# Optimization experiments

Measured on AMD Instinct MI355X. Metric: run time of the kernel, lower is better.

Reference implementation:

```python
import jax, jax.numpy as jnp
import numpy as np

E, K, IN_DIM, OUT_DIM = 100000, 16, 128, 128


def _linear_init(key, out_d, in_d):
    kw, kb = jax.random.split(key)
    bound = 1.0 / np.sqrt(in_d)
    W = jax.random.uniform(kw, (out_d, in_d), minval=-bound, maxval=bound, dtype=jnp.float32)
    b = jax.random.uniform(kb, (out_d,), minval=-bound, maxval=bound, dtype=jnp.float32)
    return W, b


def setup_inputs() -> dict:
    key = jax.random.key(0)
    k_feat, k_adj, k1, k2, k3, k4 = jax.random.split(key, 6)
    edge_features = jax.random.normal(k_feat, (E, IN_DIM), dtype=jnp.float32)
    edge_adjacency = jax.random.randint(k_adj, (E, K), 0, E, dtype=jnp.int64)
    mW1, mb1 = _linear_init(k1, OUT_DIM, 2 * IN_DIM)
    mW2, mb2 = _linear_init(k2, OUT_DIM, OUT_DIM)
    uW1, ub1 = _linear_init(k3, OUT_DIM, IN_DIM + OUT_DIM)
    uW2, ub2 = _linear_init(k4, OUT_DIM, OUT_DIM)
    return {"edge_features": edge_features, "edge_adjacency": edge_adjacency,
            "mW1": mW1, "mb1": mb1, "mW2": mW2, "mb2": mb2,
            "uW1": uW1, "ub1": ub1, "uW2": ub2 * 0 + ub2 if False else uW1 * 0 + uW1 if False else uW1, "ub1_": ub1} if False else {
            "edge_features": edge_features, "edge_adjacency": edge_adjacency,
            "mW1": mW1, "mb1": mb1, "mW2": mW2, "mb2": mb2,
            "uW1": uW1, "ub1": ub1, "uW2": uW2, "ub2": ub2}


def reference(edge_features, edge_adjacency, mW1, mb1, mW2, mb2, uW1, ub1, uW2, ub2):
    D = edge_features.shape[1]
    # message_net first Linear on concat([feat_i, feat_j]) split into two halves
    # to avoid materializing the [E, K, 2D] concat tensor.
    Wi, Wj = mW1[:, :D], mW1[:, D:]                      # each [O, D]
    self_part = edge_features @ Wi.T                     # [E, O]
    nbr_feat = edge_features[edge_adjacency]             # [E, K, D] gather
    h = jax.nn.relu(self_part[:, None, :] + jnp.einsum('ekd,od->eko', nbr_feat, Wj) + mb1)
    msg = jnp.einsum('eko,po->ekp', h, mW2) + mb2        # [E, K, O]
    msg = msg.mean(axis=1)                               # mean over neighbors -> [E, O]
    # update_net on concat([feat_i, msg_i]), split likewise
    Ui, Um = uW1[:, :D], uW1[:, D:]
    u = jax.nn.relu(edge_features @ Ui.T + msg @ Um.T + ub1)
    return u @ uW2.T + ub2                               # [E, O]
```

## Files before the change

kernel.cpp:

```cpp
#include <hip/hip_runtime.h>
#include <hip/hip_bf16.h>

#define NE 100000
#define NK 16
#define ND 128
#define NTILES 6250
#define NSUP 3125

typedef __bf16 bf16_t;
typedef bf16_t bf16x8 __attribute__((ext_vector_type(8)));
typedef bf16_t bf16x4 __attribute__((ext_vector_type(4)));
typedef float f32x4 __attribute__((ext_vector_type(4)));
typedef float f32x2 __attribute__((ext_vector_type(2)));
typedef unsigned u32x2 __attribute__((ext_vector_type(2)));
typedef unsigned short u16;
typedef unsigned char u8;

__device__ __forceinline__ u16 f2bf(float f) {
  bf16_t h = (bf16_t)f;
  return __builtin_bit_cast(u16, h);
}

__device__ __forceinline__ void soft_barrier() {
  asm volatile("s_waitcnt lgkmcnt(0)" ::: "memory");
  __builtin_amdgcn_s_barrier();
}

__global__ void k_prep(const float* __restrict__ mW1, const float* __restrict__ uW1,
                       const float* __restrict__ uW2, const float* __restrict__ mW2,
                       const float* __restrict__ ub1, const float* __restrict__ mb2,
                       u16* __restrict__ Wi_b, u16* __restrict__ Wj_b,
                       u16* __restrict__ Ui_b, u16* __restrict__ Wp_b,
                       u16* __restrict__ W2_b, float* __restrict__ bp)
{
  const int o = blockIdx.x, t = threadIdx.x;
  Wi_b[o * ND + t] = f2bf(mW1[o * 256 + t]);
  Wj_b[o * ND + t] = f2bf(mW1[o * 256 + 128 + t]);
  Ui_b[o * ND + t] = f2bf(uW1[o * 256 + t]);
  W2_b[o * ND + t] = f2bf(uW2[o * ND + t]);
  float acc = 0.f;
  for (int p = 0; p < 128; ++p)
    acc += uW1[o * 256 + 128 + p] * mW2[p * 128 + t];
  Wp_b[o * ND + t] = f2bf(acc);
  if (t == 0) {
    float b = ub1[o];
    for (int p = 0; p < 128; ++p) b += uW1[o * 256 + 128 + p] * mb2[p];
    bp[o] = b;
  }
}

__global__ __launch_bounds__(512) void k1_szt(
    const float* __restrict__ X, const u16* __restrict__ Wi_b,
    const u16* __restrict__ Wj_b, const u16* __restrict__ Ui_b,
    const float* __restrict__ mb1, const float* __restrict__ bp,
    u8* __restrict__ Sf8, u8* __restrict__ Zf8, u16* __restrict__ Tp)
{
  __shared__ u16 xt[2][16 * ND];
  __shared__ u8  eS[2][16 * ND];
  __shared__ u8  eZ[2][16 * ND];
  __shared__ u16 eT[2][16 * ND];
  const int tid = threadIdx.x, wid = tid >> 6, lane = tid & 63;
  const int r = lane & 15, q = lane >> 4;

  bf16x8 wiF[4], wjF[4], uiF[4];
  f32x4 mbF, bpF;
  {
    const int row = wid * 16 + r;
#pragma unroll
    for (int kk = 0; kk < 4; ++kk) {
      wiF[kk] = *(const bf16x8*)(Wi_b + row * ND + kk * 32 + q * 8);
      wjF[kk] = *(const bf16x8*)(Wj_b + row * ND + kk * 32 + q * 8);
      uiF[kk] = *(const bf16x8*)(Ui_b + row * ND + kk * 32 + q * 8);
    }
    mbF = *(const f32x4*)(mb1 + wid * 16 + q * 4);
    bpF = *(const f32x4*)(bp  + wid * 16 + q * 4);
  }

  const int rs = tid >> 5, cs = tid & 31;
  const int stb = rs * 256 + ((((cs >> 1) ^ (rs & 15)) << 4) | ((cs & 1) << 3));
  const int ewb = r * 256 + ((((wid * 2 + (q >> 1)) ^ (r & 15)) << 4) | ((q & 1) << 3));
  const int ezb = r * 128 + (((wid ^ (r & 7)) << 4) | (q * 4));
  const int erow = tid >> 5, c8 = tid & 31;
  const int erb = erow * 256 + ((((c8 >> 1) ^ (erow & 15)) << 4) | ((c8 & 1) << 3));
  const int zrb = erow * 128 + ((((c8 >> 2) ^ (erow & 7)) << 4) | ((c8 & 3) << 2));

  const long stride = gridDim.x;
  long t = blockIdx.x;
  if (t >= NTILES) return;

  f32x4 xr;
  auto gload = [&](long tt) {
    xr = *(const f32x4*)(X + (tt * 16 + rs) * ND + cs * 4);
  };
  auto stage = [&](int bb) {
    bf16x4 b;
#pragma unroll
    for (int i = 0; i < 4; ++i) b[i] = (bf16_t)xr[i];
    *(bf16x4*)((char*)xt[bb] + stb) = b;
  };

  gload(t);
  stage(0);
  {
    const long t1 = t + stride;
    if (t1 < NTILES) gload(t1);
  }
  soft_barrier();
  int b = 0;

  for (; t < NTILES; t += stride) {
    const long tn = t + stride, tn2 = tn + stride;

    bf16x8 xf[4];
#pragma unroll
    for (int kk = 0; kk < 4; ++kk)
      xf[kk] = *(const bf16x8*)((const char*)xt[b] +
               r * 256 + (((kk * 4 + q) ^ (r & 15)) << 4));

    if (tn < NTILES) stage(b ^ 1);
    if (tn2 < NTILES) gload(tn2);

    f32x4 aS = {0.f, 0.f, 0.f, 0.f};
    f32x4 aZ = {0.f, 0.f, 0.f, 0.f};
    f32x4 aT = {0.f, 0.f, 0.f, 0.f};
#pragma unroll
    for (int kk = 0; kk < 4; ++kk) {
      aS = __builtin_amdgcn_mfma_f32_16x16x32_bf16(wiF[kk], xf[kk], aS, 0, 0, 0);
      aZ = __builtin_amdgcn_mfma_f32_16x16x32_bf16(wjF[kk], xf[kk], aZ, 0, 0, 0);
      aT = __builtin_amdgcn_mfma_f32_16x16x32_bf16(uiF[kk], xf[kk], aT, 0, 0, 0);
    }

    bf16x4 pT;
#pragma unroll
    for (int i = 0; i < 4; ++i) pT[i] = (bf16_t)(aT[i] + bpF[i]);
    unsigned spk = 0, zpk = 0;
    spk = __builtin_amdgcn_cvt_pk_fp8_f32(aS[0] + mbF[0], aS[1] + mbF[1], spk, false);
    spk = __builtin_amdgcn_cvt_pk_fp8_f32(aS[2] + mbF[2], aS[3] + mbF[3], spk, true);
    zpk = __builtin_amdgcn_cvt_pk_fp8_f32(aZ[0], aZ[1], zpk, false);
    zpk = __builtin_amdgcn_cvt_pk_fp8_f32(aZ[2], aZ[3], zpk, true);
    *(unsigned*)((char*)eS[b] + ezb) = spk;
    *(unsigned*)((char*)eZ[b] + ezb) = zpk;
    *(bf16x4*)((char*)eT[b] + ewb) = pT;

    soft_barrier();

    {
      const long e = t * 16 + erow;
      const unsigned vS = *(const unsigned*)((const char*)eS[b] + zrb);
      const unsigned vZ = *(const unsigned*)((const char*)eZ[b] + zrb);
      const bf16x4 vT = *(const bf16x4*)((const char*)eT[b] + erb);
      *(unsigned*)(Sf8 + e * ND + c8 * 4) = vS;
      *(unsigned*)(Zf8 + e * ND + c8 * 4) = vZ;
      *(bf16x4*)(Tp + t * 2048 + erow * 128 + c8 * 4) = vT;
    }
    b ^= 1;
  }
}

__global__ __launch_bounds__(512) void k23_fused(
    const u8* __restrict__ Zf8, const u8* __restrict__ Sf8,
    const int* __restrict__ adj, const u16* __restrict__ Tp,
    const u16* __restrict__ Wp_b, const u16* __restrict__ W2_b,
    const float* __restrict__ ub2, float* __restrict__ out)
{
  __shared__ u16 ht[32 * ND];
  __shared__ u16 tt[32 * ND];
  __shared__ u16 ut[32 * ND];
  const int tid = threadIdx.x, wid = tid >> 6, lane = tid & 63;
  const int r = lane & 15, q = lane >> 4;
  const int ew = wid * 4 + q;
  const int c0 = r * 8;

  bf16x8 wpF[4], w2F[4];
  f32x4 ubF;
  {
    const int row = wid * 16 + r;
#pragma unroll
    for (int kk = 0; kk < 4; ++kk) {
      wpF[kk] = *(const bf16x8*)(Wp_b + row * ND + kk * 32 + q * 8);
      w2F[kk] = *(const bf16x8*)(W2_b + row * ND + kk * 32 + q * 8);
    }
    ubF = *(const f32x4*)(ub2 + wid * 16 + q * 4);
  }

  const int hwb = ew * 256 + ((r ^ (ew & 15)) << 4);
  const int trow = tid >> 4, tch = tid & 15;
  const int twb = trow * 256 + ((tch ^ (trow & 15)) << 4);
  const int uwb0 = (((wid * 2 + (q >> 1)) ^ r) << 4) | ((q & 1) << 3);

  const long stride = gridDim.x;
  long s = blockIdx.x;
  if (s >= NSUP) return;

  auto adjload = [&](long ss) { return adj[(ss * 32 + ew) * NK + r]; };

  int myidxN;
  float hacc[8];
  bf16x8 trC;
  {
    const int myidxC = adjload(s);
    const unsigned* sp = (const unsigned*)(Sf8 + (s * 32 + ew) * ND + c0);
    const unsigned sw0 = sp[0], sw1 = sp[1];
    trC = *(const bf16x8*)(Tp + s * 4096 + trow * 128 + tch * 8);
    const long s1 = s + stride;
    myidxN = (s1 < NSUP) ? adjload(s1) : 0;

    const f32x2 a0 = __builtin_amdgcn_cvt_pk_f32_fp8(sw0, false);
    const f32x2 a1 = __builtin_amdgcn_cvt_pk_f32_fp8(sw0, true);
    const f32x2 a2 = __builtin_amdgcn_cvt_pk_f32_fp8(sw1, false);
    const f32x2 a3 = __builtin_amdgcn_cvt_pk_f32_fp8(sw1, true);
    const float sv[8] = {a0[0], a0[1], a1[0], a1[1], a2[0], a2[1], a3[0], a3[1]};
#pragma unroll
    for (int i = 0; i < 8; ++i) hacc[i] = 0.f;
#pragma unroll
    for (int k = 0; k < NK; ++k) {
      const int n = __shfl(myidxC, (lane & 48) + k);
      const u32x2 zw = *(const u32x2*)(Zf8 + (long)n * ND + c0);
      const f32x2 z0 = __builtin_amdgcn_cvt_pk_f32_fp8(zw[0], false);
      const f32x2 z1 = __builtin_amdgcn_cvt_pk_f32_fp8(zw[0], true);
      const f32x2 z2 = __builtin_amdgcn_cvt_pk_f32_fp8(zw[1], false);
      const f32x2 z3 = __builtin_amdgcn_cvt_pk_f32_fp8(zw[1], true);
      hacc[0] += fmaxf(sv[0] + z0[0], 0.f);
      hacc[1] += fmaxf(sv[1] + z0[1], 0.f);
      hacc[2] += fmaxf(sv[2] + z1[0], 0.f);
      hacc[3] += fmaxf(sv[3] + z1[1], 0.f);
      hacc[4] += fmaxf(sv[4] + z2[0], 0.f);
      hacc[5] += fmaxf(sv[5] + z2[1], 0.f);
      hacc[6] += fmaxf(sv[6] + z3[0], 0.f);
      hacc[7] += fmaxf(sv[7] + z3[1], 0.f);
    }
  }

  for (; s < NSUP; s += stride) {
    const long sn = s + stride, sn2 = sn + stride;
    const bool hasN = (sn < NSUP);

    {
      bf16x8 hv;
#pragma unroll
      for (int i = 0; i < 8; ++i) hv[i] = (bf16_t)(hacc[i] * 0.0625f);
      *(bf16x8*)((char*)ht + hwb) = hv;
      *(bf16x8*)((char*)tt + twb) = trC;
    }

    u32x2 zbufA[8], zbufB[8];
    unsigned swn0 = 0, swn1 = 0;
    bf16x8 trN = {};
    int myidxN2 = 0;
    if (hasN) {
#pragma unroll
      for (int k = 0; k < 8; ++k) {
        const int n = __shfl(myidxN, (lane & 48) + k);
        zbufA[k] = *(const u32x2*)(Zf8 + (long)n * ND + c0);
      }
      const unsigned* sp = (const unsigned*)(Sf8 + (sn * 32 + ew) * ND + c0);
      swn0 = sp[0]; swn1 = sp[1];
      trN = *(const bf16x8*)(Tp + sn * 4096 + trow * 128 + tch * 8);
      if (sn2 < NSUP) myidxN2 = adjload(sn2);
    }

    soft_barrier();

#pragma unroll
    for (int t2 = 0; t2 < 2; ++t2) {
      const int rowb = (t2 * 16 + r) * 256;
      bf16x8 hf[4];
#pragma unroll
      for (int kk = 0; kk < 4; ++kk)
        hf[kk] = *(const bf16x8*)((const char*)ht + rowb + (((kk * 4 + q) ^ r) << 4));
      f32x4 acc;
      {
        const bf16x4 tv = *(const bf16x4*)((const char*)tt + rowb + uwb0);
#pragma unroll
        for (int i = 0; i < 4; ++i) acc[i] = (float)tv[i];
      }
#pragma unroll
      for (int kk = 0; kk < 4; ++kk)
        acc = __builtin_amdgcn_mfma_f32_16x16x32_bf16(wpF[kk], hf[kk], acc, 0, 0, 0);
      bf16x4 u;
#pragma unroll
      for (int i = 0; i < 4; ++i) u[i] = (bf16_t)fmaxf(acc[i], 0.f);
      *(bf16x4*)((char*)ut + rowb + uwb0) = u;
    }

    if (hasN) {
#pragma unroll
      for (int k = 0; k < 8; ++k) {
        const int n = __shfl(myidxN, (lane & 48) + 8 + k);
        zbufB[k] = *(const u32x2*)(Zf8 + (long)n * ND + c0);
      }
    }

    soft_barrier();

#pragma unroll
    for (int t2 = 0; t2 < 2; ++t2) {
      const int rowb = (t2 * 16 + r) * 256;
      bf16x8 uf[4];
#pragma unroll
      for (int kk = 0; kk < 4; ++kk)
        uf[kk] = *(const bf16x8*)((const char*)ut + rowb + (((kk * 4 + q) ^ r) << 4));
      f32x4 o = {0.f, 0.f, 0.f, 0.f};
#pragma unroll
      for (int kk = 0; kk < 4; ++kk)
        o = __builtin_amdgcn_mfma_f32_16x16x32_bf16(w2F[kk], uf[kk], o, 0, 0, 0);
#pragma unroll
      for (int i = 0; i < 4; ++i) o[i] += ubF[i];
      *(f32x4*)(out + (s * 32 + t2 * 16 + r) * ND + wid * 16 + q * 4) = o;
    }

    if (hasN) {
      const f32x2 a0 = __builtin_amdgcn_cvt_pk_f32_fp8(swn0, false);
      const f32x2 a1 = __builtin_amdgcn_cvt_pk_f32_fp8(swn0, true);
      const f32x2 a2 = __builtin_amdgcn_cvt_pk_f32_fp8(swn1, false);
      const f32x2 a3 = __builtin_amdgcn_cvt_pk_f32_fp8(swn1, true);
      const float sv[8] = {a0[0], a0[1], a1[0], a1[1], a2[0], a2[1], a3[0], a3[1]};
#pragma unroll
      for (int i = 0; i < 8; ++i) hacc[i] = 0.f;
#pragma unroll
      for (int k = 0; k < 16; ++k) {
        const u32x2 zw = (k < 8) ? zbufA[k] : zbufB[k - 8];
        const f32x2 z0 = __builtin_amdgcn_cvt_pk_f32_fp8(zw[0], false);
        const f32x2 z1 = __builtin_amdgcn_cvt_pk_f32_fp8(zw[0], true);
        const f32x2 z2 = __builtin_amdgcn_cvt_pk_f32_fp8(zw[1], false);
        const f32x2 z3 = __builtin_amdgcn_cvt_pk_f32_fp8(zw[1], true);
        hacc[0] += fmaxf(sv[0] + z0[0], 0.f);
        hacc[1] += fmaxf(sv[1] + z0[1], 0.f);
        hacc[2] += fmaxf(sv[2] + z1[0], 0.f);
        hacc[3] += fmaxf(sv[3] + z1[1], 0.f);
        hacc[4] += fmaxf(sv[4] + z2[0], 0.f);
        hacc[5] += fmaxf(sv[5] + z2[1], 0.f);
        hacc[6] += fmaxf(sv[6] + z3[0], 0.f);
        hacc[7] += fmaxf(sv[7] + z3[1], 0.f);
      }
      myidxN = myidxN2;
      trC = trN;
    }
  }
}

extern "C" void kernel_launch(void* const* d_in, const int* in_sizes, int n_in,
                              void* d_out, int out_size, void* d_ws, size_t ws_size,
                              hipStream_t stream)
{
  (void)in_sizes; (void)n_in; (void)out_size; (void)ws_size;
  const float* X   = (const float*)d_in[0];
  const int*   adj = (const int*)d_in[1];
  const float* mW1 = (const float*)d_in[2];
  const float* mb1 = (const float*)d_in[3];
  const float* mW2 = (const float*)d_in[4];
  const float* mb2 = (const float*)d_in[5];
  const float* uW1 = (const float*)d_in[6];
  const float* ub1 = (const float*)d_in[7];
  const float* uW2 = (const float*)d_in[8];
  const float* ub2 = (const float*)d_in[9];
  float* out = (float*)d_out;

  u8* ws8  = (u8*)d_ws;
  u8* Sf8  = ws8;
  u8* Zf8  = Sf8 + (size_t)NE * ND;
  u16* Tp  = (u16*)(Zf8 + (size_t)NE * ND);
  u16* Wi_b = Tp + (size_t)NE * ND;
  u16* Wj_b = Wi_b + 128 * 128;
  u16* Ui_b = Wj_b + 128 * 128;
  u16* Wp_b = Ui_b + 128 * 128;
  u16* W2_b = Wp_b + 128 * 128;
  float* bp = (float*)(W2_b + 128 * 128);

  k_prep<<<128, 128, 0, stream>>>(mW1, uW1, uW2, mW2, ub1, mb2,
                                  Wi_b, Wj_b, Ui_b, Wp_b, W2_b, bp);

  k1_szt<<<1024, 512, 0, stream>>>(X, Wi_b, Wj_b, Ui_b, mb1, bp, Sf8, Zf8, Tp);

  k23_fused<<<1024, 512, 0, stream>>>(Zf8, Sf8, adj, Tp, Wp_b, W2_b, ub2, out);
}
```

Before: 87.54 us.

## Store T in MFMA fragment layout, drop LDS staging, split gather buffers

The producer kernel now writes the T tensor already permuted into the MFMA accumulator layout. The fused kernel can then load each lane's T fragment straight from global memory and no longer stages it through a shared-memory tile, which removes one LDS array and its write/read traffic. The neighbour gather is restructured to use a single 8-entry buffer that is consumed in two halves, lowering register pressure, and the accumulation is vectorised into f32x4. Launch bounds are set to 6 waves per SIMD and the grid drops to 768 blocks for occupancy, at the risk of different latency hiding and a permuted-layout correctness dependency between the two kernels.

```diff
diff --git a/kernel.cpp b/kernel.cpp
--- a/kernel.cpp
+++ b/kernel.cpp
@@ -24,6 +24,35 @@
 __device__ __forceinline__ void soft_barrier() {
   asm volatile("s_waitcnt lgkmcnt(0)" ::: "memory");
   __builtin_amdgcn_s_barrier();
+}
+
+__device__ __forceinline__ void unpack_s(unsigned w0, unsigned w1,
+                                         f32x4& sA, f32x4& sB) {
+  const f32x2 a0 = __builtin_amdgcn_cvt_pk_f32_fp8(w0, false);
+  const f32x2 a1 = __builtin_amdgcn_cvt_pk_f32_fp8(w0, true);
+  const f32x2 a2 = __builtin_amdgcn_cvt_pk_f32_fp8(w1, false);
+  const f32x2 a3 = __builtin_amdgcn_cvt_pk_f32_fp8(w1, true);
+  sA[0] = a0[0]; sA[1] = a0[1]; sA[2] = a1[0]; sA[3] = a1[1];
+  sB[0] = a2[0]; sB[1] = a2[1]; sB[2] = a3[0]; sB[3] = a3[1];
+}
+
+__device__ __forceinline__ void acc8(f32x4& hA, f32x4& hB,
+                                     const f32x4 sA, const f32x4 sB,
+                                     const u32x2 zw) {
+  const f32x2 z0 = __builtin_amdgcn_cvt_pk_f32_fp8(zw[0], false);
+  const f32x2 z1 = __builtin_amdgcn_cvt_pk_f32_fp8(zw[0], true);
+  const f32x2 z2 = __builtin_amdgcn_cvt_pk_f32_fp8(zw[1], false);
+  const f32x2 z3 = __builtin_amdgcn_cvt_pk_f32_fp8(zw[1], true);
+  f32x4 vA = sA, vB = sB;
+  vA[0] += z0[0]; vA[1] += z0[1]; vA[2] += z1[0]; vA[3] += z1[1];
+  vB[0] += z2[0]; vB[1] += z2[1]; vB[2] += z3[0]; vB[3] += z3[1];
+#pragma unroll
+  for (int i = 0; i < 4; ++i) {
+    vA[i] = fmaxf(vA[i], 0.f);
+    vB[i] = fmaxf(vB[i], 0.f);
+  }
+  hA += vA;
+  hB += vB;
 }
 
 __global__ void k_prep(const float* __restrict__ mW1, const float* __restrict__ uW1,
@@ -83,6 +112,8 @@
   const int erow = tid >> 5, c8 = tid & 31;
   const int erb = erow * 256 + ((((c8 >> 1) ^ (erow & 15)) << 4) | ((c8 & 1) << 3));
   const int zrb = erow * 128 + ((((c8 >> 2) ^ (erow & 7)) << 4) | ((c8 & 3) << 2));
+  const int trb2 = (tid & 15) * 256 +
+                   ((((tid >> 5) ^ (tid & 15)) << 4) | (((tid >> 4) & 1) << 3));
 
   const long stride = gridDim.x;
   long t = blockIdx.x;
@@ -148,23 +179,22 @@
       const long e = t * 16 + erow;
       const unsigned vS = *(const unsigned*)((const char*)eS[b] + zrb);
       const unsigned vZ = *(const unsigned*)((const char*)eZ[b] + zrb);
-      const bf16x4 vT = *(const bf16x4*)((const char*)eT[b] + erb);
+      const bf16x4 vT = *(const bf16x4*)((const char*)eT[b] + trb2);
       *(unsigned*)(Sf8 + e * ND + c8 * 4) = vS;
       *(unsigned*)(Zf8 + e * ND + c8 * 4) = vZ;
-      *(bf16x4*)(Tp + t * 2048 + erow * 128 + c8 * 4) = vT;
+      *(bf16x4*)(Tp + t * 2048 + tid * 4) = vT;
     }
     b ^= 1;
   }
 }
 
-__global__ __launch_bounds__(512) void k23_fused(
+__global__ __launch_bounds__(512, 6) void k23_fused(
     const u8* __restrict__ Zf8, const u8* __restrict__ Sf8,
     const int* __restrict__ adj, const u16* __restrict__ Tp,
     const u16* __restrict__ Wp_b, const u16* __restrict__ W2_b,
     const float* __restrict__ ub2, float* __restrict__ out)
 {
   __shared__ u16 ht[32 * ND];
-  __shared__ u16 tt[32 * ND];
   __shared__ u16 ut[32 * ND];
   const int tid = threadIdx.x, wid = tid >> 6, lane = tid & 63;
   const int r = lane & 15, q = lane >> 4;
@@ -184,9 +214,8 @@
   }
 
   const int hwb = ew * 256 + ((r ^ (ew & 15)) << 4);
-  const int trow = tid >> 4, tch = tid & 15;
-  const int twb = trow * 256 + ((tch ^ (trow & 15)) << 4);
   const int uwb0 = (((wid * 2 + (q >> 1)) ^ r) << 4) | ((q & 1) << 3);
+  const int tpo = wid * 256 + q * 64 + r * 4;
 
   const long stride = gridDim.x;
   long s = blockIdx.x;
@@ -195,40 +224,33 @@
   auto adjload = [&](long ss) { return adj[(ss * 32 + ew) * NK + r]; };
 
   int myidxN;
-  float hacc[8];
-  bf16x8 trC;
+  f32x4 haccA = {0.f, 0.f, 0.f, 0.f}, haccB = {0.f, 0.f, 0.f, 0.f};
+  bf16x4 trC0, trC1;
   {
     const int myidxC = adjload(s);
     const unsigned* sp = (const unsigned*)(Sf8 + (s * 32 + ew) * ND + c0);
     const unsigned sw0 = sp[0], sw1 = sp[1];
-    trC = *(const bf16x8*)(Tp + s * 4096 + trow * 128 + tch * 8);
-    const long s1 = s + stride;
-    myidxN = (s1 < NSUP) ? adjload(s1) : 0;
-
-    const f32x2 a0 = __builtin_amdgcn_cvt_pk_f32_fp8(sw0, false);
-    const f32x2 a1 = __builtin_amdgcn_cvt_pk_f32_fp8(sw0, true);
-    const f32x2 a2 = __builtin_amdgcn_cvt_pk_f32_fp8(sw1, false);
-    const f32x2 a3 = __builtin_amdgcn_cvt_pk_f32_fp8(sw1, true);
-    const float sv[8] = {a0[0], a0[1], a1[0], a1[1], a2[0], a2[1], a3[0], a3[1]};
-#pragma unroll
-    for (int i = 0; i < 8; ++i) hacc[i] = 0.f;
-#pragma unroll
-    for (int k = 0; k < NK; ++k) {
+    trC0 = *(const bf16x4*)(Tp + s * 4096 + tpo);
+    trC1 = *(const bf16x4*)(Tp + s * 4096 + 2048 + tpo);
+    myidxN = (s + stride < NSUP) ? adjload(s + stride) : 0;
+
+    f32x4 sA, sB;
+    unpack_s(sw0, sw1, sA, sB);
+    u32x2 zb[8];
+#pragma unroll
+    for (int k = 0; k < 8; ++k) {
       const int n = __shfl(myidxC, (lane & 48) + k);
-      const u32x2 zw = *(const u32x2*)(Zf8 + (long)n * ND + c0);
-      const f32x2 z0 = __builtin_amdgcn_cvt_pk_f32_fp8(zw[0], false);
-      const f32x2 z1 = __builtin_amdgcn_cvt_pk_f32_fp8(zw[0], true);
-      const f32x2 z2 = __builtin_amdgcn_cvt_pk_f32_fp8(zw[1], false);
-      const f32x2 z3 = __builtin_amdgcn_cvt_pk_f32_fp8(zw[1], true);
-      hacc[0] += fmaxf(sv[0] + z0[0], 0.f);
-      hacc[1] += fmaxf(sv[1] + z0[1], 0.f);
-      hacc[2] += fmaxf(sv[2] + z1[0], 0.f);
-      hacc[3] += fmaxf(sv[3] + z1[1], 0.f);
-      hacc[4] += fmaxf(sv[4] + z2[0], 0.f);
-      hacc[5] += fmaxf(sv[5] + z2[1], 0.f);
-      hacc[6] += fmaxf(sv[6] + z3[0], 0.f);
-      hacc[7] += fmaxf(sv[7] + z3[1], 0.f);
-    }
+      zb[k] = *(const u32x2*)(Zf8 + (long)n * ND + c0);
+    }
+#pragma unroll
+    for (int k = 0; k < 8; ++k) acc8(haccA, haccB, sA, sB, zb[k]);
+#pragma unroll
+    for (int k = 0; k < 8; ++k) {
+      const int n = __shfl(myidxC, (lane & 48) + 8 + k);
+      zb[k] = *(const u32x2*)(Zf8 + (long)n * ND + c0);
+    }
+#pragma unroll
+    for (int k = 0; k < 8; ++k) acc8(haccA, haccB, sA, sB, zb[k]);
   }
 
   for (; s < NSUP; s += stride) {
@@ -238,25 +260,28 @@
     {
       bf16x8 hv;
 #pragma unroll
-      for (int i = 0; i < 8; ++i) hv[i] = (bf16_t)(hacc[i] * 0.0625f);
+      for (int i = 0; i < 4; ++i) {
+        hv[i]     = (bf16_t)(haccA[i] * 0.0625f);
+        hv[i + 4] = (bf16_t)(haccB[i] * 0.0625f);
+      }
       *(bf16x8*)((char*)ht + hwb) = hv;
-      *(bf16x8*)((char*)tt + twb) = trC;
-    }
-
-    u32x2 zbufA[8], zbufB[8];
+    }
+
+    u32x2 zbuf[8];
     unsigned swn0 = 0, swn1 = 0;
-    bf16x8 trN = {};
+    bf16x4 trN0 = {}, trN1 = {};
     int myidxN2 = 0;
     if (hasN) {
+      const unsigned* sp = (const unsigned*)(Sf8 + (sn * 32 + ew) * ND + c0);
+      swn0 = sp[0]; swn1 = sp[1];
+      trN0 = *(const bf16x4*)(Tp + sn * 4096 + tpo);
+      trN1 = *(const bf16x4*)(Tp + sn * 4096 + 2048 + tpo);
+      if (sn2 < NSUP) myidxN2 = adjload(sn2);
 #pragma unroll
       for (int k = 0; k < 8; ++k) {
         const int n = __shfl(myidxN, (lane & 48) + k);
-        zbufA[k] = *(const u32x2*)(Zf8 + (long)n * ND + c0);
+        zbuf[k] = *(const u32x2*)(Zf8 + (long)n * ND + c0);
       }
-      const unsigned* sp = (const unsigned*)(Sf8 + (sn * 32 + ew) * ND + c0);
-      swn0 = sp[0]; swn1 = sp[1];
-      trN = *(const bf16x8*)(Tp + sn * 4096 + trow * 128 + tch * 8);
-      if (sn2 < NSUP) myidxN2 = adjload(sn2);
     }
 
     soft_barrier();
@@ -268,12 +293,10 @@
 #pragma unroll
       for (int kk = 0; kk < 4; ++kk)
         hf[kk] = *(const bf16x8*)((const char*)ht + rowb + (((kk * 4 + q) ^ r) << 4));
+      const bf16x4 tv = t2 ? trC1 : trC0;
       f32x4 acc;
-      {
-        const bf16x4 tv = *(const bf16x4*)((const char*)tt + rowb + uwb0);
-#pragma unroll
-        for (int i = 0; i < 4; ++i) acc[i] = (float)tv[i];
-      }
+#pragma unroll
+      for (int i = 0; i < 4; ++i) acc[i] = (float)tv[i];
 #pragma unroll
       for (int kk = 0; kk < 4; ++kk)
         acc = __builtin_amdgcn_mfma_f32_16x16x32_bf16(wpF[kk], hf[kk], acc, 0, 0, 0);
@@ -283,11 +306,17 @@
       *(bf16x4*)((char*)ut + rowb + uwb0) = u;
     }
 
+    f32x4 sA, sB;
     if (hasN) {
+      unpack_s(swn0, swn1, sA, sB);
+      haccA = f32x4{0.f, 0.f, 0.f, 0.f};
+      haccB = f32x4{0.f, 0.f, 0.f, 0.f};
+#pragma unroll
+      for (int k = 0; k < 8; ++k) acc8(haccA, haccB, sA, sB, zbuf[k]);
 #pragma unroll
       for (int k = 0; k < 8; ++k) {
         const int n = __shfl(myidxN, (lane & 48) + 8 + k);
-        zbufB[k] = *(const u32x2*)(Zf8 + (long)n * ND + c0);
+        zbuf[k] = *(const u32x2*)(Zf8 + (long)n * ND + c0);
       }
     }
 
@@ -310,31 +339,11 @@
     }
 
     if (hasN) {
-      const f32x2 a0 = __builtin_amdgcn_cvt_pk_f32_fp8(swn0, false);
-      const f32x2 a1 = __builtin_amdgcn_cvt_pk_f32_fp8(swn0, true);
-      const f32x2 a2 = __builtin_amdgcn_cvt_pk_f32_fp8(swn1, false);
-      const f32x2 a3 = __builtin_amdgcn_cvt_pk_f32_fp8(swn1, true);
-      const float sv[8] = {a0[0], a0[1], a1[0], a1[1], a2[0], a2[1], a3[0], a3[1]};
-#pragma unroll
-      for (int i = 0; i < 8; ++i) hacc[i] = 0.f;
-#pragma unroll
-      for (int k = 0; k < 16; ++k) {
-        const u32x2 zw = (k < 8) ? zbufA[k] : zbufB[k - 8];
-        const f32x2 z0 = __builtin_amdgcn_cvt_pk_f32_fp8(zw[0], false);
-        const f32x2 z1 = __builtin_amdgcn_cvt_pk_f32_fp8(zw[0], true);
-        const f32x2 z2 = __builtin_amdgcn_cvt_pk_f32_fp8(zw[1], false);
-        const f32x2 z3 = __builtin_amdgcn_cvt_pk_f32_fp8(zw[1], true);
-        hacc[0] += fmaxf(sv[0] + z0[0], 0.f);
-        hacc[1] += fmaxf(sv[1] + z0[1], 0.f);
-        hacc[2] += fmaxf(sv[2] + z1[0], 0.f);
-        hacc[3] += fmaxf(sv[3] + z1[1], 0.f);
-        hacc[4] += fmaxf(sv[4] + z2[0], 0.f);
-        hacc[5] += fmaxf(sv[5] + z2[1], 0.f);
-        hacc[6] += fmaxf(sv[6] + z3[0], 0.f);
-        hacc[7] += fmaxf(sv[7] + z3[1], 0.f);
-      }
+#pragma unroll
+      for (int k = 0; k < 8; ++k) acc8(haccA, haccB, sA, sB, zbuf[k]);
       myidxN = myidxN2;
-      trC = trN;
+      trC0 = trN0;
+      trC1 = trN1;
     }
   }
 }
@@ -372,5 +381,5 @@
 
   k1_szt<<<1024, 512, 0, stream>>>(X, Wi_b, Wj_b, Ui_b, mb1, bp, Sf8, Zf8, Tp);
 
-  k23_fused<<<1024, 512, 0, stream>>>(Zf8, Sf8, adj, Tp, Wp_b, W2_b, ub2, out);
-}
+  k23_fused<<<768, 512, 0, stream>>>(Zf8, Sf8, adj, Tp, Wp_b, W2_b, ub2, out);
+}
```

Result: slower. 158.9 us (+81.5%).
